# Performance work log

Measured on AMD Instinct MI355X. Metric: run time of the kernel, lower is better.

## Reference

```python
import jax, jax.numpy as jnp
import numpy as np
from jax import lax

# Fixed high-pass biquad coefficients from SpecTransform.__init__ (a0=b0=1)
A_HP = (-1.99599, 0.996)
B_HP = (-2.0, 1.0)


def _biquad(x, b0, b1, b2, a1, a2):
    """Direct-form-I second-order IIR along last axis of x: (B, T).
    y[t] = b0*x[t] + b1*x[t-1] + b2*x[t-2] - a1*y[t-1] - a2*y[t-2]
    Matches torchaudio.functional.biquad (which calls lfilter with
    default clamp=True, clipping the final output to [-1, 1]).
    """
    z = jnp.zeros((x.shape[0],), x.dtype)

    def step(carry, xt):
        x1, x2, y1, y2 = carry
        y = b0 * xt + b1 * x1 + b2 * x2 - a1 * y1 - a2 * y2
        return (xt, x1, y, y1), y

    _, y = lax.scan(step, (z, z, z, z), x.T)  # scan over time, carry over batch
    return jnp.clip(y.T, -1.0, 1.0)


def _chain(sig, coefs):
    # coefs = [a1, a2, b1, b2] from _rand_resp (hoisted out for determinism)
    a1, a2, b1, b2 = coefs[0], coefs[1], coefs[2], coefs[3]
    sig = _biquad(sig, 1.0, B_HP[0], B_HP[1], A_HP[0], A_HP[1])
    sig = _biquad(sig, 1.0, b1, b2, a1, a2)
    return sig


def setup_inputs() -> dict:
    key = jax.random.key(0)
    k1, k2, k3, k4 = jax.random.split(key, 4)
    B, T = 64, 160000  # 64 clips of 10 s @ 16 kHz
    x = jax.random.normal(k1, (B, T), jnp.float32) * 0.1
    n = jax.random.normal(k2, (B, T), jnp.float32) * 0.1
    # 0.75 * (U[0,1) - 0.5), same distribution as _rand_resp
    coef_x = (jax.random.uniform(k3, (4,), jnp.float32) - 0.5) * 0.75
    coef_n = (jax.random.uniform(k4, (4,), jnp.float32) - 0.5) * 0.75
    return {"x": x, "n": n, "coef_x": coef_x, "coef_n": coef_n}


def reference(x, n, coef_x, coef_n):
    return (_chain(x, coef_x), _chain(n, coef_n))
```

## Files before the change

kernel.cpp:

```cpp
#include <hip/hip_runtime.h>
#include <math.h>

#define T_LEN   160000
#define NROW    128
#define CH      32
#define NCH     5000
#define OWNT    20
#define OWN_W   62
#define B_OWN   (4 * OWN_W)
#define TILES   21
#define NBLK    (NROW * TILES)

#define C1_HP ( 1.99599)
#define C2_HP (-0.996)
#define C1F   ( 1.99599f)
#define C2F   (-0.996f)

#define S1_FLOAT2S (NROW * NCH)
#define M2_BYTE_OFF (S1_FLOAT2S * 8)

#define GLOBAL_AS __attribute__((address_space(1)))
#define SHARED_AS __attribute__((address_space(3)))

__device__ __forceinline__ int swzf(int F) { return F ^ ((F >> 3) & 7); }
__device__ __forceinline__ float clip1f(float v) { return fminf(fmaxf(v, -1.0f), 1.0f); }

__global__ __launch_bounds__(256) void pass_a1(const float* __restrict__ x,
                                               const float* __restrict__ nn,
                                               float2* __restrict__ e1,
                                               const float* __restrict__ cx,
                                               const float* __restrict__ cn,
                                               float4* __restrict__ m2) {
  int g = blockIdx.x * blockDim.x + threadIdx.x;
  if (g < 2) {
    const float* c = g ? cn : cx;
    const float A1c = c[0], A2c = c[1];
    float pm2 = 0.f, pm1 = 0.f, p0 = 1.f;
#pragma unroll
    for (int k = 0; k < CH; ++k) {
      float pn = -A1c * p0 - A2c * pm1;
      pm2 = pm1; pm1 = p0; p0 = pn;
    }
    m2[g] = make_float4(p0, -A2c * pm1, pm1, -A2c * pm2);
  }
  if (g >= NROW * NCH) return;
  int row = g / NCH, c = g % NCH;
  const float* src = (row < 64) ? (x + (size_t)row * T_LEN)
                                : (nn + (size_t)(row - 64) * T_LEN);
  const float* xp = src + c * CH;
  float x1 = 0.f, x2 = 0.f;
  if (c) { x1 = xp[-1]; x2 = xp[-2]; }
  double y1 = 0.0, y2 = 0.0;
#pragma unroll
  for (int j = 0; j < CH; j += 4) {
    float4 xv = *reinterpret_cast<const float4*>(xp + j);
#define A1STEP(XF) { float xt = (XF); \
    float fir = (xt - 2.f * x1 + x2); \
    double y = fma(C1_HP, y1, fma(C2_HP, y2, (double)fir)); \
    x2 = x1; x1 = xt; y2 = y1; y1 = y; }
    A1STEP(xv.x) A1STEP(xv.y) A1STEP(xv.z) A1STEP(xv.w)
#undef A1STEP
  }
  e1[g] = make_float2((float)y1, (float)y2);
}

__global__ __launch_bounds__(256) void scan_row(const float2* __restrict__ e,
                                                float2* __restrict__ s) {
  __shared__ double wm[4][6];
  const int t = threadIdx.x, row = blockIdx.x;
  const int lane = t & 63, wv = t >> 6;
  double pm2 = 0.0, pm1 = 0.0, p0 = 1.0;
#pragma unroll
  for (int k = 1; k <= CH; ++k) {
    double pn = C1_HP * p0 + C2_HP * pm1;
    pm2 = pm1; pm1 = p0; p0 = pn;
  }
  const double m00 = p0,  m01 = C2_HP * pm1;
  const double m10 = pm1, m11 = C2_HP * pm2;
  const float2* ep = e + (size_t)row * NCH;
  const int base = t * OWNT;
  double f1 = 0.0, f2 = 0.0;
  for (int j = 0; j < OWNT; ++j) {
    int c = base + j;
    float2 ev = (c < NCH) ? ep[c] : make_float2(0.f, 0.f);
    double n1 = m00 * f1 + m01 * f2 + (double)ev.x;
    double n2 = m10 * f1 + m11 * f2 + (double)ev.y;
    f1 = n1; f2 = n2;
  }
  double b00 = m00, b01 = m01, b10 = m10, b11 = m11;
  double r00 = 1.0, r01 = 0.0, r10 = 0.0, r11 = 1.0;
  int ee = OWNT;
  while (ee) {
    if (ee & 1) {
      double t00 = b00 * r00 + b01 * r10, t01 = b00 * r01 + b01 * r11;
      double t10 = b10 * r00 + b11 * r10, t11 = b10 * r01 + b11 * r11;
      r00 = t00; r01 = t01; r10 = t10; r11 = t11;
    }
    double q00 = b00 * b00 + b01 * b10, q01 = b00 * b01 + b01 * b11;
    double q10 = b10 * b00 + b11 * b10, q11 = b10 * b01 + b11 * b11;
    b00 = q00; b01 = q01; b10 = q10; b11 = q11;
    ee >>= 1;
  }
  double P00 = r00, P01 = r01, P10 = r10, P11 = r11, V1 = f1, V2 = f2;
#pragma unroll
  for (int off = 1; off < 64; off <<= 1) {
    double u00 = __shfl_up(P00, off), u01 = __shfl_up(P01, off);
    double u10 = __shfl_up(P10, off), u11 = __shfl_up(P11, off);
    double uv1 = __shfl_up(V1, off),  uv2 = __shfl_up(V2, off);
    if (lane >= off) {
      double nv1 = P00 * uv1 + P01 * uv2 + V1;
      double nv2 = P10 * uv1 + P11 * uv2 + V2;
      double n00 = P00 * u00 + P01 * u10, n01 = P00 * u01 + P01 * u11;
      double n10 = P10 * u00 + P11 * u10, n11 = P10 * u01 + P11 * u11;
      P00 = n00; P01 = n01; P10 = n10; P11 = n11; V1 = nv1; V2 = nv2;
    }
  }
  if (lane == 63) {
    wm[wv][0] = P00; wm[wv][1] = P01; wm[wv][2] = P10; wm[wv][3] = P11;
    wm[wv][4] = V1;  wm[wv][5] = V2;
  }
  __syncthreads();
  double S1 = 0.0, S2 = 0.0;
  for (int w = 0; w < wv; ++w) {
    double n1 = wm[w][0] * S1 + wm[w][1] * S2 + wm[w][4];
    double n2 = wm[w][2] * S1 + wm[w][3] * S2 + wm[w][5];
    S1 = n1; S2 = n2;
  }
  double q00 = __shfl_up(P00, 1), q01 = __shfl_up(P01, 1);
  double q10 = __shfl_up(P10, 1), q11 = __shfl_up(P11, 1);
  double qv1 = __shfl_up(V1, 1),  qv2 = __shfl_up(V2, 1);
  double st1, st2;
  if (lane == 0) { st1 = S1; st2 = S2; }
  else { st1 = q00 * S1 + q01 * S2 + qv1; st2 = q10 * S1 + q11 * S2 + qv2; }
  float2* sp = s + (size_t)row * NCH;
  double s1v = st1, s2v = st2;
  for (int j = 0; j < OWNT; ++j) {
    int c = base + j;
    if (c < NCH) {
      sp[c] = make_float2((float)s1v, (float)s2v);
      float2 ev = ep[c];
      double n1 = m00 * s1v + m01 * s2v + (double)ev.x;
      double n2 = m10 * s1v + m11 * s2v + (double)ev.y;
      s1v = n1; s2v = n2;
    }
  }
}

__global__ __launch_bounds__(256, 5) void emit_kernel(const float* __restrict__ x,
                                                      const float* __restrict__ nn,
                                                      const float2* __restrict__ s1,
                                                      const float* __restrict__ cx,
                                                      const float* __restrict__ cn,
                                                      const float4* __restrict__ m2,
                                                      float* __restrict__ out) {
  __shared__ float4 ws4[2048];
  const int tid = threadIdx.x, lane = tid & 63, wv = tid >> 6;
  const int b = blockIdx.x;
  const int row = b / TILES, tile = b % TILES;
  const int wave_c0 = tile * B_OWN + wv * OWN_W;
  const int cb = wave_c0 - 2 + lane;
  const float* src = (row < 64) ? x + (size_t)row * T_LEN
                                : nn + (size_t)(row - 64) * T_LEN;
  const float4* src4 = reinterpret_cast<const float4*>(src);
  const float2* srow = s1 + (size_t)row * NCH;
  const float* cf = (row < 64) ? cx : cn;
  const float A1c = cf[0], A2c = cf[1], B1c = cf[2], B2c = cf[3];
  const float4 M2 = m2[(row < 64) ? 0 : 1];
  const bool valid = (cb >= 0) && (cb < NCH);

  float sy1 = 0.f, sy2 = 0.f;
  if (valid && cb > 0) { float2 sv = srow[cb]; sy1 = sv.x; sy2 = sv.y; }
  float t0x = 0.f, t0y = 0.f;
  if (lane == 0 && valid && cb > 0) {
    float2 tp = *reinterpret_cast<const float2*>(src + (long)cb * CH - 2);
    t0y = tp.x; t0x = tp.y;
  }

  const int WOFF = wv * 512;
  const long base4 = (long)(wave_c0 - 2) * 8;
  const bool interior = (base4 >= 0) && (base4 + 512 <= (long)NCH * 8);

  if (interior) {
    const int lane_swz = lane ^ ((lane >> 3) & 7);
#pragma unroll
    for (int q = 0; q < 8; ++q) {
      const float4* gp = src4 + base4 + q * 64 + lane_swz;
      __builtin_amdgcn_global_load_lds(
          (const GLOBAL_AS void*)gp,
          (SHARED_AS void*)(ws4 + WOFF + q * 64),
          16, 0, 0);
    }
    asm volatile("s_waitcnt vmcnt(0)" ::: "memory");
  } else {
#pragma unroll
    for (int q = 0; q < 8; ++q) {
      int f = q * 64 + lane;
      long g4 = base4 + f;
      float4 v = make_float4(0.f, 0.f, 0.f, 0.f);
      if (g4 >= 0 && g4 < (long)NCH * 8)
        v = src4[g4];
      ws4[WOFF + swzf(f)] = v;
    }
  }

  float4 a[8];
#pragma unroll
  for (int q = 0; q < 8; ++q) a[q] = ws4[WOFF + swzf(lane * 8 + q)];

  float tx = __shfl_up(a[7].w, 1);
  float ty = __shfl_up(a[7].z, 1);

  float x1, x2, y1, y2, v1, v2;
  if (valid && cb > 0) {
    y1 = sy1; y2 = sy2;
    v1 = clip1f(sy1); v2 = clip1f(sy2);
    if (lane == 0) { x1 = t0x; x2 = t0y; }
    else { x1 = tx; x2 = ty; }
  } else { x1 = 0.f; x2 = 0.f; y1 = 0.f; y2 = 0.f; v1 = 0.f; v2 = 0.f; }

  {
    float xp1 = x1, xp2 = x2;
#pragma unroll
    for (int q = 0; q < 8; ++q) {
      float4 t = a[q];
      float4 f;
      f.x = t.x - 2.f * xp1 + xp2;
      f.y = t.y - 2.f * t.x + xp1;
      f.z = t.z - 2.f * t.y + t.x;
      f.w = t.w - 2.f * t.z + t.y;
      xp2 = t.z; xp1 = t.w;
      a[q] = f;
    }
  }

  float z1 = 0.f, z2 = 0.f;
  if (valid) {
#define AB(REF) { \
    float yy = fmaf(C1F, y1, fmaf(C2F, y2, (REF))); \
    float vv = clip1f(yy); \
    float zz = fmaf(-A1c, z1, fmaf(-A2c, z2, fmaf(B2c, v2, fmaf(B1c, v1, vv)))); \
    y2 = y1; y1 = yy; v2 = v1; v1 = vv; z2 = z1; z1 = zz; REF = zz; }
#pragma unroll
    for (int q = 0; q < 8; ++q) { AB(a[q].x) AB(a[q].y) AB(a[q].z) AB(a[q].w) }
#undef AB
  }

  float u1x = __shfl_up(z1, 1), u1y = __shfl_up(z2, 1);
  float u2x = __shfl_up(z1, 2), u2y = __shfl_up(z2, 2);

  if (lane >= 2 && valid) {
    float s2x, s2y;
    if (cb == 0)      { s2x = 0.f; s2y = 0.f; }
    else if (cb == 1) { s2x = u1x; s2y = u1y; }
    else {
      s2x = fmaf(M2.x, u2x, fmaf(M2.y, u2y, u1x));
      s2y = fmaf(M2.z, u2x, fmaf(M2.w, u2y, u1y));
    }
    float h1 = s2x, h2 = s2y;
#define CS(ZB, OT) { float hh = fmaf(-A1c, h1, -A2c * h2); \
    OT = clip1f((ZB) + hh); h2 = h1; h1 = hh; }
#pragma unroll
    for (int q = 0; q < 8; ++q) {
      float4 o;
      CS(a[q].x, o.x) CS(a[q].y, o.y) CS(a[q].z, o.z) CS(a[q].w, o.w)
      ws4[WOFF + swzf(lane * 8 + q)] = o;
    }
#undef CS
  }

  float* orow = out + (size_t)row * T_LEN;
#pragma unroll
  for (int q = 0; q < 8; ++q) {
    int f = q * 64 + lane;
    long g4 = base4 + f;
    if (f >= 16 && g4 < (long)NCH * 8)
      reinterpret_cast<float4*>(orow)[g4] = ws4[WOFF + swzf(f)];
  }
}

extern "C" void kernel_launch(void* const* d_in, const int* in_sizes, int n_in,
                              void* d_out, int out_size, void* d_ws, size_t ws_size,
                              hipStream_t stream) {
  const float* x  = (const float*)d_in[0];
  const float* nn = (const float*)d_in[1];
  const float* cx = (const float*)d_in[2];
  const float* cn = (const float*)d_in[3];
  float* out = (float*)d_out;

  float2* e1 = (float2*)d_out;
  float2* s1 = (float2*)d_ws;
  float4* m2 = (float4*)((char*)d_ws + M2_BYTE_OFF);

  const int total = NROW * NCH;
  const int blk = 256;
  const int nb = (total + blk - 1) / blk;

  pass_a1<<<nb, blk, 0, stream>>>(x, nn, e1, cx, cn, m2);
  scan_row<<<NROW, blk, 0, stream>>>(e1, s1);
  emit_kernel<<<NBLK, blk, 0, stream>>>(x, nn, s1, cx, cn, m2, out);
}
```

Before: 60.04 us.

## Split emit chunks to 16 samples per lane with four-step carry correction

The emit kernel now has each lane handle a 16-sample sub-chunk instead of 32, doubling the number of blocks. Each block needs half the LDS, and occupancy is raised to 8 blocks per SIMD. Odd lanes reconstruct their first-filter state by advancing 16 samples from the 32-chunk boundary state, and the second-filter carry correction now sums four preceding lanes using precomputed M, M^2 and M^3 matrices. The intent is to shorten the serial per-lane recurrence and increase parallelism. The cost is extra shuffles, extra odd-lane work and more halo overlap (4 of 64 lanes).

```diff
diff --git a/kernel.cpp b/kernel.cpp
--- a/kernel.cpp
+++ b/kernel.cpp
@@ -6,10 +6,12 @@
 #define CH      32
 #define NCH     5000
 #define OWNT    20
-#define OWN_W   62
-#define B_OWN   (4 * OWN_W)
-#define TILES   21
-#define NBLK    (NROW * TILES)
+#define NCH16   10000
+#define OWN16   60
+#define B16     240
+#define TILES16 42
+#define NBLK16  (NROW * TILES16)
+#define ROW4    40000
 
 #define C1_HP ( 1.99599)
 #define C2_HP (-0.996)
@@ -22,7 +24,7 @@
 #define GLOBAL_AS __attribute__((address_space(1)))
 #define SHARED_AS __attribute__((address_space(3)))
 
-__device__ __forceinline__ int swzf(int F) { return F ^ ((F >> 3) & 7); }
+__device__ __forceinline__ int sz16(int F) { return F ^ ((F >> 3) & 7); }
 __device__ __forceinline__ float clip1f(float v) { return fminf(fmaxf(v, -1.0f), 1.0f); }
 
 __global__ __launch_bounds__(256) void pass_a1(const float* __restrict__ x,
@@ -37,11 +39,18 @@
     const float A1c = c[0], A2c = c[1];
     float pm2 = 0.f, pm1 = 0.f, p0 = 1.f;
 #pragma unroll
-    for (int k = 0; k < CH; ++k) {
+    for (int k = 0; k < 16; ++k) {
       float pn = -A1c * p0 - A2c * pm1;
       pm2 = pm1; pm1 = p0; p0 = pn;
     }
-    m2[g] = make_float4(p0, -A2c * pm1, pm1, -A2c * pm2);
+    float m00 = p0, m01 = -A2c * pm1, m10 = pm1, m11 = -A2c * pm2;
+    float q00 = m00*m00 + m01*m10, q01 = m00*m01 + m01*m11;
+    float q10 = m10*m00 + m11*m10, q11 = m10*m01 + m11*m11;
+    float r00 = q00*m00 + q01*m10, r01 = q00*m01 + q01*m11;
+    float r10 = q10*m00 + q11*m10, r11 = q10*m01 + q11*m11;
+    m2[g*3 + 0] = make_float4(m00, m01, m10, m11);
+    m2[g*3 + 1] = make_float4(q00, q01, q10, q11);
+    m2[g*3 + 2] = make_float4(r00, r01, r10, r11);
   }
   if (g >= NROW * NCH) return;
   int row = g / NCH, c = g % NCH;
@@ -146,45 +155,38 @@
   }
 }
 
-__global__ __launch_bounds__(256, 5) void emit_kernel(const float* __restrict__ x,
+__global__ __launch_bounds__(256, 8) void emit_kernel(const float* __restrict__ x,
                                                       const float* __restrict__ nn,
                                                       const float2* __restrict__ s1,
                                                       const float* __restrict__ cx,
                                                       const float* __restrict__ cn,
                                                       const float4* __restrict__ m2,
                                                       float* __restrict__ out) {
-  __shared__ float4 ws4[2048];
+  __shared__ float4 ws4[1024];
   const int tid = threadIdx.x, lane = tid & 63, wv = tid >> 6;
   const int b = blockIdx.x;
-  const int row = b / TILES, tile = b % TILES;
-  const int wave_c0 = tile * B_OWN + wv * OWN_W;
-  const int cb = wave_c0 - 2 + lane;
+  const int row = b / TILES16, tile = b % TILES16;
+  const int W0 = tile * B16 + wv * OWN16;
+  const int c = W0 - 4 + lane;
   const float* src = (row < 64) ? x + (size_t)row * T_LEN
                                 : nn + (size_t)(row - 64) * T_LEN;
   const float4* src4 = reinterpret_cast<const float4*>(src);
   const float2* srow = s1 + (size_t)row * NCH;
   const float* cf = (row < 64) ? cx : cn;
   const float A1c = cf[0], A2c = cf[1], B1c = cf[2], B2c = cf[3];
-  const float4 M2 = m2[(row < 64) ? 0 : 1];
-  const bool valid = (cb >= 0) && (cb < NCH);
-
-  float sy1 = 0.f, sy2 = 0.f;
-  if (valid && cb > 0) { float2 sv = srow[cb]; sy1 = sv.x; sy2 = sv.y; }
-  float t0x = 0.f, t0y = 0.f;
-  if (lane == 0 && valid && cb > 0) {
-    float2 tp = *reinterpret_cast<const float2*>(src + (long)cb * CH - 2);
-    t0y = tp.x; t0x = tp.y;
-  }
-
-  const int WOFF = wv * 512;
-  const long base4 = (long)(wave_c0 - 2) * 8;
-  const bool interior = (base4 >= 0) && (base4 + 512 <= (long)NCH * 8);
+  const int fi = (row < 64) ? 0 : 1;
+  const float4 M1q = m2[fi*3], M2q = m2[fi*3+1], M3q = m2[fi*3+2];
+  const bool cOK = (c >= 0) && (c < NCH16);
+
+  const int WOFF = wv * 256;
+  const long base4 = (long)(W0 - 4) * 4;
+  const bool interior = (base4 >= 0) && (base4 + 256 <= ROW4);
 
   if (interior) {
-    const int lane_swz = lane ^ ((lane >> 3) & 7);
-#pragma unroll
-    for (int q = 0; q < 8; ++q) {
-      const float4* gp = src4 + base4 + q * 64 + lane_swz;
+    const int lane_sz = lane ^ ((lane >> 3) & 7);
+#pragma unroll
+    for (int q = 0; q < 4; ++q) {
+      const float4* gp = src4 + base4 + q * 64 + lane_sz;
       __builtin_amdgcn_global_load_lds(
           (const GLOBAL_AS void*)gp,
           (SHARED_AS void*)(ws4 + WOFF + q * 64),
@@ -193,35 +195,61 @@
     asm volatile("s_waitcnt vmcnt(0)" ::: "memory");
   } else {
 #pragma unroll
-    for (int q = 0; q < 8; ++q) {
+    for (int q = 0; q < 4; ++q) {
       int f = q * 64 + lane;
       long g4 = base4 + f;
       float4 v = make_float4(0.f, 0.f, 0.f, 0.f);
-      if (g4 >= 0 && g4 < (long)NCH * 8)
-        v = src4[g4];
-      ws4[WOFF + swzf(f)] = v;
-    }
-  }
-
-  float4 a[8];
-#pragma unroll
-  for (int q = 0; q < 8; ++q) a[q] = ws4[WOFF + swzf(lane * 8 + q)];
-
-  float tx = __shfl_up(a[7].w, 1);
-  float ty = __shfl_up(a[7].z, 1);
-
-  float x1, x2, y1, y2, v1, v2;
-  if (valid && cb > 0) {
-    y1 = sy1; y2 = sy2;
-    v1 = clip1f(sy1); v2 = clip1f(sy2);
-    if (lane == 0) { x1 = t0x; x2 = t0y; }
-    else { x1 = tx; x2 = ty; }
-  } else { x1 = 0.f; x2 = 0.f; y1 = 0.f; y2 = 0.f; v1 = 0.f; v2 = 0.f; }
+      if (g4 >= 0 && g4 < ROW4) v = src4[g4];
+      ws4[WOFF + sz16(f)] = v;
+    }
+  }
+
+  float4 a[4];
+#pragma unroll
+  for (int q = 0; q < 4; ++q) a[q] = ws4[WOFF + sz16(lane * 4 + q)];
+
+  float tx  = __shfl_up(a[3].w, 1), ty  = __shfl_up(a[3].z, 1);
+  float t2x = __shfl_up(a[3].w, 2), t2y = __shfl_up(a[3].z, 2);
+
+  float x1 = 0.f, x2 = 0.f, y1 = 0.f, y2 = 0.f, v1 = 0.f, v2 = 0.f;
+  if (cOK && c > 0) {
+    float2 sv = srow[c >> 1];
+    y1 = sv.x; y2 = sv.y;
+    if ((lane & 1) == 0) {
+      if (lane == 0) {
+        float2 tp = *reinterpret_cast<const float2*>(src + (long)c * 16 - 2);
+        x2 = tp.x; x1 = tp.y;
+      } else { x1 = tx; x2 = ty; }
+    } else {
+      float ax1 = 0.f, ax2 = 0.f;
+      if (lane == 1) {
+        if (c >= 2) {
+          float2 tp = *reinterpret_cast<const float2*>(src + (long)(c - 1) * 16 - 2);
+          ax2 = tp.x; ax1 = tp.y;
+        }
+      } else { ax1 = t2x; ax2 = t2y; }
+      float4 p0 = ws4[WOFF + sz16((lane - 1) * 4 + 0)];
+      float4 p1 = ws4[WOFF + sz16((lane - 1) * 4 + 1)];
+      float4 p2 = ws4[WOFF + sz16((lane - 1) * 4 + 2)];
+      float4 p3 = ws4[WOFF + sz16((lane - 1) * 4 + 3)];
+#define ADV(XT) { float xt_ = (XT); \
+      float fir = (xt_ - 2.f * ax1 + ax2); \
+      float yy = fmaf(C1F, y1, fmaf(C2F, y2, fir)); \
+      ax2 = ax1; ax1 = xt_; y2 = y1; y1 = yy; }
+      ADV(p0.x) ADV(p0.y) ADV(p0.z) ADV(p0.w)
+      ADV(p1.x) ADV(p1.y) ADV(p1.z) ADV(p1.w)
+      ADV(p2.x) ADV(p2.y) ADV(p2.z) ADV(p2.w)
+      ADV(p3.x) ADV(p3.y) ADV(p3.z) ADV(p3.w)
+#undef ADV
+      x1 = ax1; x2 = ax2;
+    }
+    v1 = clip1f(y1); v2 = clip1f(y2);
+  }
 
   {
     float xp1 = x1, xp2 = x2;
 #pragma unroll
-    for (int q = 0; q < 8; ++q) {
+    for (int q = 0; q < 4; ++q) {
       float4 t = a[q];
       float4 f;
       f.x = t.x - 2.f * xp1 + xp2;
@@ -234,47 +262,50 @@
   }
 
   float z1 = 0.f, z2 = 0.f;
-  if (valid) {
+  if (cOK) {
 #define AB(REF) { \
     float yy = fmaf(C1F, y1, fmaf(C2F, y2, (REF))); \
     float vv = clip1f(yy); \
     float zz = fmaf(-A1c, z1, fmaf(-A2c, z2, fmaf(B2c, v2, fmaf(B1c, v1, vv)))); \
     y2 = y1; y1 = yy; v2 = v1; v1 = vv; z2 = z1; z1 = zz; REF = zz; }
 #pragma unroll
-    for (int q = 0; q < 8; ++q) { AB(a[q].x) AB(a[q].y) AB(a[q].z) AB(a[q].w) }
+    for (int q = 0; q < 4; ++q) { AB(a[q].x) AB(a[q].y) AB(a[q].z) AB(a[q].w) }
 #undef AB
   }
 
   float u1x = __shfl_up(z1, 1), u1y = __shfl_up(z2, 1);
   float u2x = __shfl_up(z1, 2), u2y = __shfl_up(z2, 2);
-
-  if (lane >= 2 && valid) {
-    float s2x, s2y;
-    if (cb == 0)      { s2x = 0.f; s2y = 0.f; }
-    else if (cb == 1) { s2x = u1x; s2y = u1y; }
-    else {
-      s2x = fmaf(M2.x, u2x, fmaf(M2.y, u2y, u1x));
-      s2y = fmaf(M2.z, u2x, fmaf(M2.w, u2y, u1y));
-    }
+  float u3x = __shfl_up(z1, 3), u3y = __shfl_up(z2, 3);
+  float u4x = __shfl_up(z1, 4), u4y = __shfl_up(z2, 4);
+
+  if (lane >= 4 && cOK) {
+    float s2x = 0.f, s2y = 0.f;
+    if (c >= 1) { s2x = u1x; s2y = u1y; }
+    if (c >= 2) { s2x = fmaf(M1q.x, u2x, fmaf(M1q.y, u2y, s2x));
+                  s2y = fmaf(M1q.z, u2x, fmaf(M1q.w, u2y, s2y)); }
+    if (c >= 3) { s2x = fmaf(M2q.x, u3x, fmaf(M2q.y, u3y, s2x));
+                  s2y = fmaf(M2q.z, u3x, fmaf(M2q.w, u3y, s2y)); }
+    if (c >= 4) { s2x = fmaf(M3q.x, u4x, fmaf(M3q.y, u4y, s2x));
+                  s2y = fmaf(M3q.z, u4x, fmaf(M3q.w, u4y, s2y)); }
     float h1 = s2x, h2 = s2y;
 #define CS(ZB, OT) { float hh = fmaf(-A1c, h1, -A2c * h2); \
     OT = clip1f((ZB) + hh); h2 = h1; h1 = hh; }
 #pragma unroll
-    for (int q = 0; q < 8; ++q) {
+    for (int q = 0; q < 4; ++q) {
       float4 o;
       CS(a[q].x, o.x) CS(a[q].y, o.y) CS(a[q].z, o.z) CS(a[q].w, o.w)
-      ws4[WOFF + swzf(lane * 8 + q)] = o;
+      ws4[WOFF + sz16(lane * 4 + q)] = o;
     }
 #undef CS
   }
 
   float* orow = out + (size_t)row * T_LEN;
 #pragma unroll
-  for (int q = 0; q < 8; ++q) {
+  for (int q = 0; q < 4; ++q) {
     int f = q * 64 + lane;
     long g4 = base4 + f;
-    if (f >= 16 && g4 < (long)NCH * 8)
-      reinterpret_cast<float4*>(orow)[g4] = ws4[WOFF + swzf(f)];
+    if (f >= 16 && g4 < ROW4)
+      reinterpret_cast<float4*>(orow)[g4] = ws4[WOFF + sz16(f)];
   }
 }
 
@@ -297,5 +328,5 @@
 
   pass_a1<<<nb, blk, 0, stream>>>(x, nn, e1, cx, cn, m2);
   scan_row<<<NROW, blk, 0, stream>>>(e1, s1);
-  emit_kernel<<<NBLK, blk, 0, stream>>>(x, nn, s1, cx, cn, m2, out);
+  emit_kernel<<<NBLK16, blk, 0, stream>>>(x, nn, s1, cx, cn, m2, out);
 }
```

Result: slower. 62.91 us (+4.8%).

## Fuse three-pass biquad scan into single-pass kernel with decoupled look-back

Applied to the files above, without the earlier changes.

Replaces the three launches (chunk-local pass, per-row scan, emit) with one fused kernel. Each block computes its chunk-local high-pass states in registers, combines them across waves, publishes a tile aggregate with flag-based release/acquire, and looks back at earlier tiles of the same row through an atomic ticket ordering. This removes the intermediate global round trips and reads the input once instead of twice. In exchange it adds inter-block spin-waiting, a serial look-back over up to 20 tiles per block, and recovers the first lanes' states by inverting the transition matrix, which may be numerically sensitive.

```diff
diff --git a/kernel.cpp b/kernel.cpp
--- a/kernel.cpp
+++ b/kernel.cpp
@@ -5,70 +5,121 @@
 #define NROW    128
 #define CH      32
 #define NCH     5000
-#define OWNT    20
 #define OWN_W   62
 #define B_OWN   (4 * OWN_W)
 #define TILES   21
 #define NBLK    (NROW * TILES)
+#define ROW4    40000
+#define NSTATE  (NBLK + 1)
 
 #define C1_HP ( 1.99599)
 #define C2_HP (-0.996)
 #define C1F   ( 1.99599f)
 #define C2F   (-0.996f)
 
-#define S1_FLOAT2S (NROW * NCH)
-#define M2_BYTE_OFF (S1_FLOAT2S * 8)
-
 #define GLOBAL_AS __attribute__((address_space(1)))
 #define SHARED_AS __attribute__((address_space(3)))
 
 __device__ __forceinline__ int swzf(int F) { return F ^ ((F >> 3) & 7); }
 __device__ __forceinline__ float clip1f(float v) { return fminf(fmaxf(v, -1.0f), 1.0f); }
 
-__global__ __launch_bounds__(256) void pass_a1(const float* __restrict__ x,
-                                               const float* __restrict__ nn,
-                                               float2* __restrict__ e1,
-                                               const float* __restrict__ cx,
-                                               const float* __restrict__ cn,
-                                               float4* __restrict__ m2) {
-  int g = blockIdx.x * blockDim.x + threadIdx.x;
-  if (g < 2) {
-    const float* c = g ? cn : cx;
-    const float A1c = c[0], A2c = c[1];
-    float pm2 = 0.f, pm1 = 0.f, p0 = 1.f;
-#pragma unroll
-    for (int k = 0; k < CH; ++k) {
-      float pn = -A1c * p0 - A2c * pm1;
-      pm2 = pm1; pm1 = p0; p0 = pn;
-    }
-    m2[g] = make_float4(p0, -A2c * pm1, pm1, -A2c * pm2);
-  }
-  if (g >= NROW * NCH) return;
-  int row = g / NCH, c = g % NCH;
-  const float* src = (row < 64) ? (x + (size_t)row * T_LEN)
-                                : (nn + (size_t)(row - 64) * T_LEN);
-  const float* xp = src + c * CH;
-  float x1 = 0.f, x2 = 0.f;
-  if (c) { x1 = xp[-1]; x2 = xp[-2]; }
-  double y1 = 0.0, y2 = 0.0;
-#pragma unroll
-  for (int j = 0; j < CH; j += 4) {
-    float4 xv = *reinterpret_cast<const float4*>(xp + j);
-#define A1STEP(XF) { float xt = (XF); \
-    float fir = (xt - 2.f * x1 + x2); \
-    double y = fma(C1_HP, y1, fma(C2_HP, y2, (double)fir)); \
-    x2 = x1; x1 = xt; y2 = y1; y1 = y; }
-    A1STEP(xv.x) A1STEP(xv.y) A1STEP(xv.z) A1STEP(xv.w)
-#undef A1STEP
-  }
-  e1[g] = make_float2((float)y1, (float)y2);
+__global__ void init_kernel(unsigned* __restrict__ st) {
+  int i = blockIdx.x * blockDim.x + threadIdx.x;
+  if (i < NSTATE) st[i] = 0u;
 }
 
-__global__ __launch_bounds__(256) void scan_row(const float2* __restrict__ e,
-                                                float2* __restrict__ s) {
-  __shared__ double wm[4][6];
-  const int t = threadIdx.x, row = blockIdx.x;
-  const int lane = t & 63, wv = t >> 6;
+__global__ __launch_bounds__(256, 4) void fused_kernel(
+    const float* __restrict__ x, const float* __restrict__ nn,
+    const float* __restrict__ cx, const float* __restrict__ cn,
+    double* __restrict__ pay, unsigned* __restrict__ st,
+    unsigned* __restrict__ ticket, float* __restrict__ out) {
+  __shared__ float4 ws4[2048];
+  __shared__ double wmS[4][6];
+  __shared__ double SinS[2];
+  __shared__ unsigned vidS;
+
+  const int tid = threadIdx.x, lane = tid & 63, wv = tid >> 6;
+  if (tid == 0) vidS = atomicAdd(ticket, 1u);
+  __syncthreads();
+  const unsigned vid = vidS;
+  const int row = vid / TILES, tile = vid % TILES;
+
+  const float* src = (row < 64) ? x + (size_t)row * T_LEN
+                                : nn + (size_t)(row - 64) * T_LEN;
+  const float4* src4 = reinterpret_cast<const float4*>(src);
+  const float* cf = (row < 64) ? cx : cn;
+  const float A1c = cf[0], A2c = cf[1], B1c = cf[2], B2c = cf[3];
+
+  const int wave_c0 = tile * B_OWN + wv * OWN_W;
+  const int cb = wave_c0 - 2 + lane;
+  const bool valid = (cb >= 0) && (cb < NCH);
+  const int WOFF = wv * 512;
+  const long base4 = (long)(wave_c0 - 2) * 8;
+  const bool interior = (base4 >= 0) && (base4 + 512 <= (long)ROW4);
+
+  float2 tp = make_float2(0.f, 0.f);
+  if (lane == 0 && valid && cb > 0)
+    tp = *reinterpret_cast<const float2*>(src + (long)cb * CH - 2);
+
+  if (interior) {
+    const int lane_sz = lane ^ ((lane >> 3) & 7);
+#pragma unroll
+    for (int q = 0; q < 8; ++q)
+      __builtin_amdgcn_global_load_lds(
+          (const GLOBAL_AS void*)(src4 + base4 + q * 64 + lane_sz),
+          (SHARED_AS void*)(ws4 + WOFF + q * 64), 16, 0, 0);
+    asm volatile("s_waitcnt vmcnt(0)" ::: "memory");
+  } else {
+#pragma unroll
+    for (int q = 0; q < 8; ++q) {
+      int f = q * 64 + lane;
+      long g4 = base4 + f;
+      float4 v = make_float4(0.f, 0.f, 0.f, 0.f);
+      if (g4 >= 0 && g4 < ROW4) v = src4[g4];
+      ws4[WOFF + swzf(f)] = v;
+    }
+  }
+
+  float4 a[8];
+#pragma unroll
+  for (int q = 0; q < 8; ++q) a[q] = ws4[WOFF + swzf(lane * 8 + q)];
+
+  float tx = __shfl_up(a[7].w, 1), ty = __shfl_up(a[7].z, 1);
+  float x1i, x2i;
+  if (valid && cb > 0) {
+    if (lane == 0) { x1i = tp.y; x2i = tp.x; }
+    else { x1i = tx; x2i = ty; }
+  } else { x1i = 0.f; x2i = 0.f; }
+
+  double ey1 = 0.0, ey2 = 0.0;
+  {
+    float xx1 = x1i, xx2 = x2i;
+#pragma unroll
+    for (int q = 0; q < 8; ++q) {
+#define E1S(XF) { float xt = (XF); \
+      float fir = (xt - 2.f * xx1 + xx2); \
+      double yv = fma(C1_HP, ey1, fma(C2_HP, ey2, (double)fir)); \
+      xx2 = xx1; xx1 = xt; ey2 = ey1; ey1 = yv; }
+      E1S(a[q].x) E1S(a[q].y) E1S(a[q].z) E1S(a[q].w)
+#undef E1S
+    }
+  }
+
+  {
+    float xp1 = x1i, xp2 = x2i;
+#pragma unroll
+    for (int q = 0; q < 8; ++q) {
+      float4 t = a[q];
+      float4 f;
+      f.x = t.x - 2.f * xp1 + xp2;
+      f.y = t.y - 2.f * t.x + xp1;
+      f.z = t.z - 2.f * t.y + t.x;
+      f.w = t.w - 2.f * t.z + t.y;
+      xp2 = t.z; xp1 = t.w;
+      a[q] = f;
+    }
+  }
+
   double pm2 = 0.0, pm1 = 0.0, p0 = 1.0;
 #pragma unroll
   for (int k = 1; k <= CH; ++k) {
@@ -77,31 +128,11 @@
   }
   const double m00 = p0,  m01 = C2_HP * pm1;
   const double m10 = pm1, m11 = C2_HP * pm2;
-  const float2* ep = e + (size_t)row * NCH;
-  const int base = t * OWNT;
-  double f1 = 0.0, f2 = 0.0;
-  for (int j = 0; j < OWNT; ++j) {
-    int c = base + j;
-    float2 ev = (c < NCH) ? ep[c] : make_float2(0.f, 0.f);
-    double n1 = m00 * f1 + m01 * f2 + (double)ev.x;
-    double n2 = m10 * f1 + m11 * f2 + (double)ev.y;
-    f1 = n1; f2 = n2;
-  }
-  double b00 = m00, b01 = m01, b10 = m10, b11 = m11;
-  double r00 = 1.0, r01 = 0.0, r10 = 0.0, r11 = 1.0;
-  int ee = OWNT;
-  while (ee) {
-    if (ee & 1) {
-      double t00 = b00 * r00 + b01 * r10, t01 = b00 * r01 + b01 * r11;
-      double t10 = b10 * r00 + b11 * r10, t11 = b10 * r01 + b11 * r11;
-      r00 = t00; r01 = t01; r10 = t10; r11 = t11;
-    }
-    double q00 = b00 * b00 + b01 * b10, q01 = b00 * b01 + b01 * b11;
-    double q10 = b10 * b00 + b11 * b10, q11 = b10 * b01 + b11 * b11;
-    b00 = q00; b01 = q01; b10 = q10; b11 = q11;
-    ee >>= 1;
-  }
-  double P00 = r00, P01 = r01, P10 = r10, P11 = r11, V1 = f1, V2 = f2;
+
+  const bool inscan = (lane >= 2) && valid;
+  double P00 = inscan ? m00 : 1.0, P01 = inscan ? m01 : 0.0;
+  double P10 = inscan ? m10 : 0.0, P11 = inscan ? m11 : 1.0;
+  double V1 = inscan ? ey1 : 0.0,  V2 = inscan ? ey2 : 0.0;
 #pragma unroll
   for (int off = 1; off < 64; off <<= 1) {
     double u00 = __shfl_up(P00, off), u01 = __shfl_up(P01, off);
@@ -116,122 +147,95 @@
     }
   }
   if (lane == 63) {
-    wm[wv][0] = P00; wm[wv][1] = P01; wm[wv][2] = P10; wm[wv][3] = P11;
-    wm[wv][4] = V1;  wm[wv][5] = V2;
-  }
+    wmS[wv][0] = P00; wmS[wv][1] = P01; wmS[wv][2] = P10; wmS[wv][3] = P11;
+    wmS[wv][4] = V1;  wmS[wv][5] = V2;
+  }
+  double E00 = __shfl_up(P00, 1), E01 = __shfl_up(P01, 1);
+  double E10 = __shfl_up(P10, 1), E11 = __shfl_up(P11, 1);
+  double EV1 = __shfl_up(V1, 1),  EV2 = __shfl_up(V2, 1);
+  if (lane == 0) { E00 = 1.0; E01 = 0.0; E10 = 0.0; E11 = 1.0; EV1 = 0.0; EV2 = 0.0; }
   __syncthreads();
-  double S1 = 0.0, S2 = 0.0;
+
+  if (tid == 0) {
+    double bP00 = 1.0, bP01 = 0.0, bP10 = 0.0, bP11 = 1.0, bV1 = 0.0, bV2 = 0.0;
+#pragma unroll
+    for (int w = 0; w < 4; ++w) {
+      double w00 = wmS[w][0], w01 = wmS[w][1], w10 = wmS[w][2], w11 = wmS[w][3];
+      double wv1 = wmS[w][4], wv2 = wmS[w][5];
+      double n00 = w00 * bP00 + w01 * bP10, n01 = w00 * bP01 + w01 * bP11;
+      double n10 = w10 * bP00 + w11 * bP10, n11 = w10 * bP01 + w11 * bP11;
+      double nv1 = w00 * bV1 + w01 * bV2 + wv1;
+      double nv2 = w10 * bV1 + w11 * bV2 + wv2;
+      bP00 = n00; bP01 = n01; bP10 = n10; bP11 = n11; bV1 = nv1; bV2 = nv2;
+    }
+    double* r = pay + (size_t)vid * 6;
+    __hip_atomic_store(r + 0, bP00, __ATOMIC_RELAXED, __HIP_MEMORY_SCOPE_AGENT);
+    __hip_atomic_store(r + 1, bP01, __ATOMIC_RELAXED, __HIP_MEMORY_SCOPE_AGENT);
+    __hip_atomic_store(r + 2, bP10, __ATOMIC_RELAXED, __HIP_MEMORY_SCOPE_AGENT);
+    __hip_atomic_store(r + 3, bP11, __ATOMIC_RELAXED, __HIP_MEMORY_SCOPE_AGENT);
+    __hip_atomic_store(r + 4, bV1,  __ATOMIC_RELAXED, __HIP_MEMORY_SCOPE_AGENT);
+    __hip_atomic_store(r + 5, bV2,  __ATOMIC_RELAXED, __HIP_MEMORY_SCOPE_AGENT);
+    __hip_atomic_store(&st[vid], 1u, __ATOMIC_RELEASE, __HIP_MEMORY_SCOPE_AGENT);
+  }
+  if (wv == 0) {
+    double LP00 = 1.0, LP01 = 0.0, LP10 = 0.0, LP11 = 1.0, LV1 = 0.0, LV2 = 0.0;
+    if (lane < tile) {
+      unsigned idx = (unsigned)row * TILES + lane;
+      int guard = 0;
+      while (__hip_atomic_load(&st[idx], __ATOMIC_ACQUIRE,
+                               __HIP_MEMORY_SCOPE_AGENT) == 0u &&
+             ++guard < (1 << 25))
+        __builtin_amdgcn_s_sleep(2);
+      const double* r = pay + (size_t)idx * 6;
+      LP00 = __hip_atomic_load(r + 0, __ATOMIC_RELAXED, __HIP_MEMORY_SCOPE_AGENT);
+      LP01 = __hip_atomic_load(r + 1, __ATOMIC_RELAXED, __HIP_MEMORY_SCOPE_AGENT);
+      LP10 = __hip_atomic_load(r + 2, __ATOMIC_RELAXED, __HIP_MEMORY_SCOPE_AGENT);
+      LP11 = __hip_atomic_load(r + 3, __ATOMIC_RELAXED, __HIP_MEMORY_SCOPE_AGENT);
+      LV1  = __hip_atomic_load(r + 4, __ATOMIC_RELAXED, __HIP_MEMORY_SCOPE_AGENT);
+      LV2  = __hip_atomic_load(r + 5, __ATOMIC_RELAXED, __HIP_MEMORY_SCOPE_AGENT);
+    }
+    double S1 = 0.0, S2 = 0.0;
+    for (int j = 0; j < tile; ++j) {
+      double p00 = __shfl(LP00, j), p01 = __shfl(LP01, j);
+      double p10 = __shfl(LP10, j), p11 = __shfl(LP11, j);
+      double q1  = __shfl(LV1, j),  q2  = __shfl(LV2, j);
+      double n1 = p00 * S1 + p01 * S2 + q1;
+      double n2 = p10 * S1 + p11 * S2 + q2;
+      S1 = n1; S2 = n2;
+    }
+    if (lane == 0) { SinS[0] = S1; SinS[1] = S2; }
+  }
+  __syncthreads();
+
+  double S1 = SinS[0], S2 = SinS[1];
   for (int w = 0; w < wv; ++w) {
-    double n1 = wm[w][0] * S1 + wm[w][1] * S2 + wm[w][4];
-    double n2 = wm[w][2] * S1 + wm[w][3] * S2 + wm[w][5];
+    double n1 = wmS[w][0] * S1 + wmS[w][1] * S2 + wmS[w][4];
+    double n2 = wmS[w][2] * S1 + wmS[w][3] * S2 + wmS[w][5];
     S1 = n1; S2 = n2;
   }
-  double q00 = __shfl_up(P00, 1), q01 = __shfl_up(P01, 1);
-  double q10 = __shfl_up(P10, 1), q11 = __shfl_up(P11, 1);
-  double qv1 = __shfl_up(V1, 1),  qv2 = __shfl_up(V2, 1);
-  double st1, st2;
-  if (lane == 0) { st1 = S1; st2 = S2; }
-  else { st1 = q00 * S1 + q01 * S2 + qv1; st2 = q10 * S1 + q11 * S2 + qv2; }
-  float2* sp = s + (size_t)row * NCH;
-  double s1v = st1, s2v = st2;
-  for (int j = 0; j < OWNT; ++j) {
-    int c = base + j;
-    if (c < NCH) {
-      sp[c] = make_float2((float)s1v, (float)s2v);
-      float2 ev = ep[c];
-      double n1 = m00 * s1v + m01 * s2v + (double)ev.x;
-      double n2 = m10 * s1v + m11 * s2v + (double)ev.y;
-      s1v = n1; s2v = n2;
-    }
-  }
-}
-
-__global__ __launch_bounds__(256, 5) void emit_kernel(const float* __restrict__ x,
-                                                      const float* __restrict__ nn,
-                                                      const float2* __restrict__ s1,
-                                                      const float* __restrict__ cx,
-                                                      const float* __restrict__ cn,
-                                                      const float4* __restrict__ m2,
-                                                      float* __restrict__ out) {
-  __shared__ float4 ws4[2048];
-  const int tid = threadIdx.x, lane = tid & 63, wv = tid >> 6;
-  const int b = blockIdx.x;
-  const int row = b / TILES, tile = b % TILES;
-  const int wave_c0 = tile * B_OWN + wv * OWN_W;
-  const int cb = wave_c0 - 2 + lane;
-  const float* src = (row < 64) ? x + (size_t)row * T_LEN
-                                : nn + (size_t)(row - 64) * T_LEN;
-  const float4* src4 = reinterpret_cast<const float4*>(src);
-  const float2* srow = s1 + (size_t)row * NCH;
-  const float* cf = (row < 64) ? cx : cn;
-  const float A1c = cf[0], A2c = cf[1], B1c = cf[2], B2c = cf[3];
-  const float4 M2 = m2[(row < 64) ? 0 : 1];
-  const bool valid = (cb >= 0) && (cb < NCH);
-
-  float sy1 = 0.f, sy2 = 0.f;
-  if (valid && cb > 0) { float2 sv = srow[cb]; sy1 = sv.x; sy2 = sv.y; }
-  float t0x = 0.f, t0y = 0.f;
-  if (lane == 0 && valid && cb > 0) {
-    float2 tp = *reinterpret_cast<const float2*>(src + (long)cb * CH - 2);
-    t0y = tp.x; t0x = tp.y;
-  }
-
-  const int WOFF = wv * 512;
-  const long base4 = (long)(wave_c0 - 2) * 8;
-  const bool interior = (base4 >= 0) && (base4 + 512 <= (long)NCH * 8);
-
-  if (interior) {
-    const int lane_swz = lane ^ ((lane >> 3) & 7);
-#pragma unroll
-    for (int q = 0; q < 8; ++q) {
-      const float4* gp = src4 + base4 + q * 64 + lane_swz;
-      __builtin_amdgcn_global_load_lds(
-          (const GLOBAL_AS void*)gp,
-          (SHARED_AS void*)(ws4 + WOFF + q * 64),
-          16, 0, 0);
-    }
-    asm volatile("s_waitcnt vmcnt(0)" ::: "memory");
-  } else {
-#pragma unroll
-    for (int q = 0; q < 8; ++q) {
-      int f = q * 64 + lane;
-      long g4 = base4 + f;
-      float4 v = make_float4(0.f, 0.f, 0.f, 0.f);
-      if (g4 >= 0 && g4 < (long)NCH * 8)
-        v = src4[g4];
-      ws4[WOFF + swzf(f)] = v;
-    }
-  }
-
-  float4 a[8];
-#pragma unroll
-  for (int q = 0; q < 8; ++q) a[q] = ws4[WOFF + swzf(lane * 8 + q)];
-
-  float tx = __shfl_up(a[7].w, 1);
-  float ty = __shfl_up(a[7].z, 1);
-
-  float x1, x2, y1, y2, v1, v2;
+  double sd1 = E00 * S1 + E01 * S2 + EV1;
+  double sd2 = E10 * S1 + E11 * S2 + EV2;
+  {
+    double det = 1.0;
+#pragma unroll
+    for (int k = 0; k < CH; ++k) det *= (-C2_HP);
+    double i00 = m11 / det, i01 = -m01 / det, i10 = -m10 / det, i11 = m00 / det;
+    double e1o = __shfl(ey1, 1), e2o = __shfl(ey2, 1);
+    if (lane == 1) {
+      sd1 = i00 * (S1 - ey1) + i01 * (S2 - ey2);
+      sd2 = i10 * (S1 - ey1) + i11 * (S2 - ey2);
+    } else if (lane == 0) {
+      double t1 = i00 * (S1 - e1o) + i01 * (S2 - e2o);
+      double t2 = i10 * (S1 - e1o) + i11 * (S2 - e2o);
+      sd1 = i00 * (t1 - ey1) + i01 * (t2 - ey2);
+      sd2 = i10 * (t1 - ey1) + i11 * (t2 - ey2);
+    }
+  }
+  float y1, y2, v1, v2;
   if (valid && cb > 0) {
-    y1 = sy1; y2 = sy2;
-    v1 = clip1f(sy1); v2 = clip1f(sy2);
-    if (lane == 0) { x1 = t0x; x2 = t0y; }
-    else { x1 = tx; x2 = ty; }
-  } else { x1 = 0.f; x2 = 0.f; y1 = 0.f; y2 = 0.f; v1 = 0.f; v2 = 0.f; }
-
-  {
-    float xp1 = x1, xp2 = x2;
-#pragma unroll
-    for (int q = 0; q < 8; ++q) {
-      float4 t = a[q];
-      float4 f;
-      f.x = t.x - 2.f * xp1 + xp2;
-      f.y = t.y - 2.f * t.x + xp1;
-      f.z = t.z - 2.f * t.y + t.x;
-      f.w = t.w - 2.f * t.z + t.y;
-      xp2 = t.z; xp1 = t.w;
-      a[q] = f;
-    }
-  }
+    y1 = (float)sd1; y2 = (float)sd2;
+    v1 = clip1f(y1); v2 = clip1f(y2);
+  } else { y1 = 0.f; y2 = 0.f; v1 = 0.f; v2 = 0.f; }
 
   float z1 = 0.f, z2 = 0.f;
   if (valid) {
@@ -249,12 +253,19 @@
   float u2x = __shfl_up(z1, 2), u2y = __shfl_up(z2, 2);
 
   if (lane >= 2 && valid) {
+    float q2m = 0.f, q1m = 0.f, q0m = 1.f;
+#pragma unroll
+    for (int k = 0; k < CH; ++k) {
+      float qn = -A1c * q0m - A2c * q1m;
+      q2m = q1m; q1m = q0m; q0m = qn;
+    }
+    const float M00 = q0m, M01 = -A2c * q1m, M10 = q1m, M11 = -A2c * q2m;
     float s2x, s2y;
     if (cb == 0)      { s2x = 0.f; s2y = 0.f; }
     else if (cb == 1) { s2x = u1x; s2y = u1y; }
     else {
-      s2x = fmaf(M2.x, u2x, fmaf(M2.y, u2y, u1x));
-      s2y = fmaf(M2.z, u2x, fmaf(M2.w, u2y, u1y));
+      s2x = fmaf(M00, u2x, fmaf(M01, u2y, u1x));
+      s2y = fmaf(M10, u2x, fmaf(M11, u2y, u1y));
     }
     float h1 = s2x, h2 = s2y;
 #define CS(ZB, OT) { float hh = fmaf(-A1c, h1, -A2c * h2); \
@@ -273,7 +284,7 @@
   for (int q = 0; q < 8; ++q) {
     int f = q * 64 + lane;
     long g4 = base4 + f;
-    if (f >= 16 && g4 < (long)NCH * 8)
+    if (f >= 16 && g4 < ROW4)
       reinterpret_cast<float4*>(orow)[g4] = ws4[WOFF + swzf(f)];
   }
 }
@@ -287,15 +298,10 @@
   const float* cn = (const float*)d_in[3];
   float* out = (float*)d_out;
 
-  float2* e1 = (float2*)d_out;
-  float2* s1 = (float2*)d_ws;
-  float4* m2 = (float4*)((char*)d_ws + M2_BYTE_OFF);
-
-  const int total = NROW * NCH;
-  const int blk = 256;
-  const int nb = (total + blk - 1) / blk;
-
-  pass_a1<<<nb, blk, 0, stream>>>(x, nn, e1, cx, cn, m2);
-  scan_row<<<NROW, blk, 0, stream>>>(e1, s1);
-  emit_kernel<<<NBLK, blk, 0, stream>>>(x, nn, s1, cx, cn, m2, out);
+  double*   pay    = (double*)d_ws;
+  unsigned* st     = (unsigned*)((char*)d_ws + (size_t)NBLK * 6 * 8);
+  unsigned* ticket = st + NBLK;
+
+  init_kernel<<<(NSTATE + 255) / 256, 256, 0, stream>>>(st);
+  fused_kernel<<<NBLK, 256, 0, stream>>>(x, nn, cx, cn, pay, st, ticket, out);
 }
```

Measured after the change: 192.3 us. 3.2x slower.
